# Performance work log

Measured on AMD Instinct MI355X. Metric: run time of the kernel, lower is better.

Reference implementation:

```python
import jax, jax.numpy as jnp
import numpy as np

# ---- hyperparameters (from init_kwargs) ----
B, SEQ, D_MODEL = 2, 2048, 1024
D_STATE, D_CONV, EXPAND, HEAD_DIM, CHUNK = 128, 4, 2, 64, 256
D_INNER = EXPAND * D_MODEL            # 2048
NH = D_INNER // HEAD_DIM              # 32 heads
CONV_DIM = D_INNER + 2 * D_STATE      # 2304
D_IN_PROJ = 2 * D_INNER + 2 * D_STATE + NH  # z, xBC, dt -> 4384
D_FF = 4 * D_MODEL
EPS = 1e-12


def setup_inputs() -> dict:
    key = jax.random.key(0)
    ks = jax.random.split(key, 16)
    s = 0.02
    f32 = jnp.float32
    inp = {
        "x": jax.random.normal(ks[0], (B, SEQ, D_MODEL), f32),
        "time_diff": jax.random.uniform(ks[1], (B, SEQ), f32),
        # TiSSD (Mamba2-style) params
        "W_in": jax.random.normal(ks[2], (D_MODEL, D_IN_PROJ), f32) * s,
        "b_in": jnp.zeros((D_IN_PROJ,), f32),
        "conv_w": jax.random.normal(ks[3], (CONV_DIM, D_CONV), f32) * s,
        "conv_b": jnp.zeros((CONV_DIM,), f32),
        "A_log": jnp.log(jnp.arange(1, NH + 1, dtype=f32)),
        "dt_bias": jnp.full((NH,), -2.0, f32),
        "D": jnp.ones((NH,), f32),
        "time_decay": jnp.full((NH,), -3.0, f32),   # time-aware decay rates
        "rms_w": jnp.ones((D_INNER,), f32),
        "W_out": jax.random.normal(ks[4], (D_INNER, D_MODEL), f32) * s,
        "b_out": jnp.zeros((D_MODEL,), f32),
        # wrapper LayerNorm
        "ln_g": jnp.ones((D_MODEL,), f32),
        "ln_b": jnp.zeros((D_MODEL,), f32),
        # FFN
        "fc1_w": jax.random.normal(ks[5], (D_MODEL, D_FF), f32) * s,
        "fc1_b": jnp.zeros((D_FF,), f32),
        "fc2_w": jax.random.normal(ks[6], (D_FF, D_MODEL), f32) * s,
        "fc2_b": jnp.zeros((D_MODEL,), f32),
        "ln2_g": jnp.ones((D_MODEL,), f32),
        "ln2_b": jnp.zeros((D_MODEL,), f32),
    }
    return inp


def _layer_norm(x, g, b, eps=EPS):
    mu = jnp.mean(x, axis=-1, keepdims=True)
    var = jnp.mean(jnp.square(x - mu), axis=-1, keepdims=True)
    return (x - mu) * jax.lax.rsqrt(var + eps) * g + b


def _hardswish(x):
    return x * jnp.clip(x + 3.0, 0.0, 6.0) * (1.0 / 6.0)


def _tissd_forward(x, time_diff, W_in, b_in, conv_w, conv_b, A_log, dt_bias, D,
                   time_decay, rms_w, W_out, b_out):
    b, l, _ = x.shape
    zxbcdt = x @ W_in + b_in                       # [b,l,D_IN_PROJ]
    z = zxbcdt[..., :D_INNER]
    xBC = zxbcdt[..., D_INNER:D_INNER + CONV_DIM]
    dt_raw = zxbcdt[..., -NH:]

    # causal depthwise conv1d (small fixed kernel -> unrolled shifts)
    xp = jnp.pad(xBC, ((0, 0), (D_CONV - 1, 0), (0, 0)))
    xBC_c = conv_b
    for k in range(D_CONV):
        xBC_c = xBC_c + xp[:, k:k + l, :] * conv_w[:, k]
    xBC_c = jax.nn.silu(xBC_c)

    xs = xBC_c[..., :D_INNER]
    Bm = xBC_c[..., D_INNER:D_INNER + D_STATE]     # [b,l,n]
    Cm = xBC_c[..., -D_STATE:]                     # [b,l,n]

    dt = jax.nn.softplus(dt_raw + dt_bias)         # [b,l,h]
    A = -jnp.exp(A_log)                            # [h]
    # time-aware: extra decay proportional to time gap
    dA = dt * A - jax.nn.softplus(time_decay) * time_diff[..., None]  # [b,l,h]

    xh = xs.reshape(b, l, NH, HEAD_DIM)
    xdt = xh * dt[..., None]                       # [b,l,h,p]

    nc = l // CHUNK
    xc = xdt.reshape(b, nc, CHUNK, NH, HEAD_DIM)
    Bc = Bm.reshape(b, nc, CHUNK, D_STATE)
    Cc = Cm.reshape(b, nc, CHUNK, D_STATE)
    dAc = dA.reshape(b, nc, CHUNK, NH).transpose(0, 3, 1, 2)  # [b,h,c,L]

    A_cum = jnp.cumsum(dAc, axis=-1)               # [b,h,c,L]
    seg = A_cum[..., :, None] - A_cum[..., None, :]
    mask = jnp.tril(jnp.ones((CHUNK, CHUNK), bool))
    Lmat = jnp.where(mask, jnp.exp(jnp.where(mask, seg, 0.0)), 0.0)  # [b,h,c,L,L]

    # intra-chunk (diagonal block) output
    Y_diag = jnp.einsum("bcln,bcsn,bhcls,bcshp->bclhp", Cc, Bc, Lmat, xc)

    # per-chunk final states
    decay_states = jnp.exp(A_cum[..., -1:] - A_cum)  # [b,h,c,L]
    states = jnp.einsum("bcln,bhcl,bclhp->bchpn", Bc, decay_states, xc)
    chunk_decay = jnp.exp(A_cum[..., -1])            # [b,h,c]

    # inter-chunk recurrence over nc chunks
    states_t = states.transpose(1, 0, 2, 3, 4)       # [c,b,h,p,n]
    decay_t = chunk_decay.transpose(2, 0, 1)         # [c,b,h]

    def step(carry, inp):
        s_c, d_c = inp
        new = carry * d_c[..., None, None] + s_c
        return new, carry                            # emit state BEFORE chunk

    init = jnp.zeros((b, NH, HEAD_DIM, D_STATE), x.dtype)
    _, prev_states = jax.lax.scan(step, init, (states_t, decay_t))
    prev_states = prev_states.transpose(1, 0, 2, 3, 4)  # [b,c,h,p,n]

    state_decay = jnp.exp(A_cum)                     # [b,h,c,L]
    Y_off = jnp.einsum("bcln,bchpn,bhcl->bclhp", Cc, prev_states, state_decay)

    Y = (Y_diag + Y_off).reshape(b, l, NH, HEAD_DIM) + D[None, None, :, None] * xh
    y = Y.reshape(b, l, D_INNER)

    # gated RMSNorm
    y = y * jax.nn.silu(z)
    y = y * jax.lax.rsqrt(jnp.mean(jnp.square(y), axis=-1, keepdims=True) + EPS) * rms_w
    return y @ W_out + b_out


def reference(x, time_diff, W_in, b_in, conv_w, conv_b, A_log, dt_bias, D,
              time_decay, rms_w, W_out, b_out, ln_g, ln_b,
              fc1_w, fc1_b, fc2_w, fc2_b, ln2_g, ln2_b):
    hidden = _tissd_forward(x, time_diff, W_in, b_in, conv_w, conv_b, A_log,
                            dt_bias, D, time_decay, rms_w, W_out, b_out)
    # num_layers > 1 -> residual; dropout is identity in eval mode
    h = _layer_norm(hidden + x, ln_g, ln_b)
    # FFN with Hardswish and residual LayerNorm
    hid = _hardswish(h @ fc1_w + fc1_b)
    hid = hid @ fc2_w + fc2_b
    out = _layer_norm(hid + h, ln2_g, ln2_b)
    return (out, time_diff)
```

## Files before the change

kernel.cpp:

```cpp
#include <hip/hip_runtime.h>

#define BATCH 2
#define SEQL 2048
#define DM 1024
#define DSTATE 128
#define HD 64
#define CHUNK 256
#define DI 2048
#define NHEADS 32
#define CONVD 2304
#define DPROJ 4384
#define DFF 4096
#define NC 8
#define ROWS (BATCH*SEQL)

typedef unsigned short ushort_t;
typedef short bf16x8 __attribute__((ext_vector_type(8)));
typedef float f32x4 __attribute__((ext_vector_type(4)));

__device__ __forceinline__ float softplus_f(float v){
    return (v > 20.f) ? v : log1pf(expf(v));
}
__device__ __forceinline__ float silu_f(float v){
    return v / (1.f + expf(-v));
}
__device__ __forceinline__ ushort_t f2b(float v){
    union { float f; unsigned int u; } x; x.f = v;
    unsigned int r = x.u + 0x7fffu + ((x.u >> 16) & 1u);
    return (ushort_t)(r >> 16);
}
__device__ __forceinline__ float b2f(ushort_t v){
    union { unsigned int u; float f; } x; x.u = ((unsigned int)v) << 16;
    return x.f;
}

template<int ACT, int OUT_BF16, int TN, int NS, int DTX>
__global__ __launch_bounds__(256) void mfma_gemm_k(
    const ushort_t* __restrict__ A, const ushort_t* __restrict__ Bt,
    const float* __restrict__ bias, float* __restrict__ Cf,
    ushort_t* __restrict__ Cb, float* __restrict__ dtaux,
    int M, int N, int K, int ldc)
{
    constexpr int NT = (TN == 128) ? 4 : 2;
    constexpr int BROWS = TN / 4;
    __shared__ ushort_t As[128*64];
    __shared__ ushort_t Bs[TN*64];
    int tid = threadIdx.x;
    int lane = tid & 63, wave = tid >> 6;
    int m0 = blockIdx.y * 128, n0 = blockIdx.x * TN;
    int Ks = K / NS;
    int kb = (NS > 1) ? blockIdx.z * Ks : 0;
    int wave_m = (TN==128) ? (wave >> 1)*64 : (wave & 1)*64;
    int wave_n = (TN==128) ? (wave & 1)*64 : (wave >> 1)*32;
    int lrow = lane >> 3;
    int lcol = ((lane & 7) ^ lrow) * 8;
    const ushort_t* Abase = A  + (size_t)(m0 + wave*32    + lrow)*K + lcol + kb;
    const ushort_t* Bbase = Bt + (size_t)(n0 + wave*BROWS + lrow)*K + lcol + kb;
    ushort_t* AsW = &As[(wave*32)*64];
    ushort_t* BsW = &Bs[(wave*BROWS)*64];
    f32x4 acc[4][NT];
    #pragma unroll
    for (int i=0;i<4;i++)
        #pragma unroll
        for (int j=0;j<NT;j++) acc[i][j] = (f32x4){0.f,0.f,0.f,0.f};
    int lm = lane & 15;
    int quad = lane >> 4;
    for (int k0 = 0; k0 < Ks; k0 += 64){
        #pragma unroll
        for (int j = 0; j < 4; j++)
            __builtin_amdgcn_global_load_lds(
                (const __attribute__((address_space(1))) void*)(Abase + (size_t)(j*8)*K + k0),
                (__attribute__((address_space(3))) void*)(AsW + j*8*64), 16, 0, 0);
        #pragma unroll
        for (int j = 0; j < BROWS/8; j++)
            __builtin_amdgcn_global_load_lds(
                (const __attribute__((address_space(1))) void*)(Bbase + (size_t)(j*8)*K + k0),
                (__attribute__((address_space(3))) void*)(BsW + j*8*64), 16, 0, 0);
        __syncthreads();
        #pragma unroll
        for (int kk = 0; kk < 64; kk += 32){
            int cb = kk >> 3;
            bf16x8 af[4], bfr[NT];
            #pragma unroll
            for (int mt=0; mt<4; mt++)
                af[mt] = *(const bf16x8*)&As[(wave_m + mt*16 + lm)*64 + (((cb + quad) ^ (lm & 7))*8)];
            #pragma unroll
            for (int nt=0; nt<NT; nt++)
                bfr[nt] = *(const bf16x8*)&Bs[(wave_n + nt*16 + lm)*64 + (((cb + quad) ^ (lm & 7))*8)];
            #pragma unroll
            for (int mt=0; mt<4; mt++)
                #pragma unroll
                for (int nt=0; nt<NT; nt++)
                    acc[mt][nt] = __builtin_amdgcn_mfma_f32_16x16x32_bf16(af[mt], bfr[nt], acc[mt][nt], 0, 0, 0);
        }
        __syncthreads();
    }
    float* Cfo = Cf + (size_t)((NS > 1) ? blockIdx.z : 0) * (size_t)M * ldc;
    int addb = (NS == 1) || (blockIdx.z == 0);
    int crow0 = m0 + wave_m + quad * 4;
    int ccol0 = n0 + wave_n + lm;
    #pragma unroll
    for (int mt=0; mt<4; mt++){
        #pragma unroll
        for (int nt=0; nt<NT; nt++){
            int col = ccol0 + nt*16;
            if (col < N){
                float bv = addb ? bias[col] : 0.f;
                #pragma unroll
                for (int r=0; r<4; r++){
                    int row = crow0 + mt*16 + r;
                    float v = acc[mt][nt][r] + bv;
                    if (ACT == 1){
                        float t = fminf(fmaxf(v + 3.f, 0.f), 6.f);
                        v = v * t * (1.f/6.f);
                    }
                    if (OUT_BF16){
                        Cb[(size_t)row*ldc + col] = f2b(v);
                        if (DTX && col >= N - NHEADS)
                            dtaux[(size_t)row*NHEADS + (col - (N - NHEADS))] = v;
                    } else {
                        Cfo[(size_t)row*ldc + col] = v;
                    }
                }
            }
        }
    }
}

__global__ __launch_bounds__(256) void transpose_bf_k(const float* __restrict__ W,
                                                      ushort_t* __restrict__ Wt,
                                                      int K, int N){
    __shared__ ushort_t tile[32][33];
    int n0 = blockIdx.x*32, k0 = blockIdx.y*32;
    int tx = threadIdx.x & 31, ty = threadIdx.x >> 5;
    #pragma unroll
    for (int i = 0; i < 4; i++){
        int k = k0 + ty + i*8;
        int n = n0 + tx;
        float v = (n < N) ? W[(size_t)k*N + n] : 0.f;
        tile[ty + i*8][tx] = f2b(v);
    }
    __syncthreads();
    #pragma unroll
    for (int i = 0; i < 4; i++){
        Wt[(size_t)(n0 + ty + i*8)*K + k0 + tx] = tile[tx][ty + i*8];
    }
}

__global__ __launch_bounds__(256) void f2b_k(const float* __restrict__ in,
                                             ushort_t* __restrict__ outp, int n){
    int idx = blockIdx.x*256 + threadIdx.x;
    if (idx < n) outp[idx] = f2b(in[idx]);
}

__global__ __launch_bounds__(256) void conv_silu_k(const ushort_t* __restrict__ zx,
                                                   const float* __restrict__ conv_w,
                                                   const float* __restrict__ conv_b,
                                                   const float* __restrict__ dt,
                                                   float* __restrict__ convb,
                                                   float* __restrict__ xdt){
    int idx = blockIdx.x*256 + threadIdx.x;
    int c = idx % CONVD;
    int row = idx / CONVD;
    int t = row & (SEQL-1);
    float acc = conv_b[c];
    #pragma unroll
    for (int k = 0; k < 4; k++){
        int tt = t + k - 3;
        if (tt >= 0)
            acc += b2f(zx[((size_t)(row + k - 3))*DPROJ + DI + c]) * conv_w[c*4 + k];
    }
    float v = silu_f(acc);
    convb[idx] = v;
    if (c < DI)
        xdt[(size_t)row*DI + c] = v * dt[(size_t)row*NHEADS + (c >> 6)];
}

__global__ __launch_bounds__(256) void dt_scan_k(const float* __restrict__ dtaux,
                                                 const float* __restrict__ time_diff,
                                                 const float* __restrict__ A_log,
                                                 const float* __restrict__ dt_bias,
                                                 const float* __restrict__ time_decay,
                                                 float* __restrict__ dt_out,
                                                 float* __restrict__ Acum){
    __shared__ float s[CHUNK];
    int bid = blockIdx.x;
    int c = bid % NC;
    int h = (bid / NC) % NHEADS;
    int b = bid / (NC*NHEADS);
    int l = threadIdx.x;
    int t = c*CHUNK + l;
    float dtr = dtaux[((size_t)(b*SEQL + t))*NHEADS + h];
    float dtv = softplus_f(dtr + dt_bias[h]);
    float A = -expf(A_log[h]);
    float dA = dtv*A - softplus_f(time_decay[h]) * time_diff[b*SEQL + t];
    dt_out[(size_t)(b*SEQL + t)*NHEADS + h] = dtv;
    s[l] = dA;
    __syncthreads();
    for (int off = 1; off < CHUNK; off <<= 1){
        float v = (l >= off) ? s[l-off] : 0.f;
        __syncthreads();
        s[l] += v;
        __syncthreads();
    }
    Acum[((size_t)(b*NHEADS + h))*SEQL + t] = s[l];
}

__global__ __launch_bounds__(256) void g_mfma_k(const float* __restrict__ convb,
                                                float* __restrict__ G){
    __shared__ ushort_t As[64*136];
    __shared__ ushort_t Bs[64*136];
    int bc = blockIdx.z;
    int l0 = blockIdx.y*64, s0 = blockIdx.x*64;
    int tid = threadIdx.x;
    int lane = tid & 63, wave = tid >> 6;
    int lm = lane & 15, quad = lane >> 4;
    const float* base = convb + (size_t)bc*CHUNK*CONVD;
    #pragma unroll
    for (int i = 0; i < 32; i++){
        int e = tid + i*256; int r = e >> 7, k = e & 127;
        As[r*136 + k] = f2b(base[(size_t)(l0+r)*CONVD + DI + DSTATE + k]);
        Bs[r*136 + k] = f2b(base[(size_t)(s0+r)*CONVD + DI + k]);
    }
    __syncthreads();
    f32x4 acc[4];
    #pragma unroll
    for (int j=0;j<4;j++) acc[j] = (f32x4){0.f,0.f,0.f,0.f};
    #pragma unroll
    for (int kk = 0; kk < 4; kk++){
        bf16x8 af = *(const bf16x8*)&As[(wave*16+lm)*136 + kk*32 + quad*8];
        #pragma unroll
        for (int nt = 0; nt < 4; nt++){
            bf16x8 bfr = *(const bf16x8*)&Bs[(nt*16+lm)*136 + kk*32 + quad*8];
            acc[nt] = __builtin_amdgcn_mfma_f32_16x16x32_bf16(af, bfr, acc[nt], 0, 0, 0);
        }
    }
    float* g = G + (size_t)bc*CHUNK*CHUNK;
    #pragma unroll
    for (int nt = 0; nt < 4; nt++)
        #pragma unroll
        for (int r = 0; r < 4; r++)
            g[(size_t)(l0 + wave*16 + quad*4 + r)*CHUNK + s0 + nt*16 + lm] = acc[nt][r];
}

#define RSX 264
#define RSB 72
__global__ __launch_bounds__(256) void states_mfma_k(const float* __restrict__ convb,
                                                     const float* __restrict__ xdt,
                                                     const float* __restrict__ Acum,
                                                     float* __restrict__ states){
    __shared__ ushort_t xw[64*RSX];
    __shared__ ushort_t Bt[128*RSB];
    __shared__ float Acs[CHUNK];
    int bid = blockIdx.x;
    int h = bid % NHEADS;
    int c = (bid / NHEADS) % NC;
    int b = bid / (NHEADS*NC);
    int tid = threadIdx.x;
    int lane = tid & 63, wave = tid >> 6;
    int lm = lane & 15, quad = lane >> 4;
    Acs[tid] = Acum[((size_t)(b*NHEADS + h))*SEQL + c*CHUNK + tid];
    __syncthreads();
    float AcL = Acs[CHUNK-1];
    {
        const float* xg = xdt + ((size_t)(b*SEQL + c*CHUNK))*DI + h*HD;
        #pragma unroll
        for (int j8 = 0; j8 < 8; j8++){
            int s0 = wave*64 + j8*8;
            bf16x8 pk;
            #pragma unroll
            for (int j = 0; j < 8; j++)
                pk[j] = (short)f2b(expf(AcL - Acs[s0+j]) * xg[(size_t)(s0+j)*DI + lane]);
            *(bf16x8*)&xw[lane*RSX + s0] = pk;
        }
    }
    f32x4 acc[8];
    #pragma unroll
    for (int j=0;j<8;j++) acc[j] = (f32x4){0.f,0.f,0.f,0.f};
    const float* bbase = convb + ((size_t)(b*SEQL + c*CHUNK))*CONVD + DI;
    for (int l0 = 0; l0 < CHUNK; l0 += 64){
        __syncthreads();
        #pragma unroll
        for (int i = 0; i < 32; i++){
            int e = tid + i*256; int l = e >> 7, n = e & 127;
            Bt[n*RSB + l] = f2b(bbase[(size_t)(l0+l)*CONVD + n]);
        }
        __syncthreads();
        #pragma unroll
        for (int kk = 0; kk < 2; kk++){
            bf16x8 af = *(const bf16x8*)&xw[(wave*16+lm)*RSX + l0 + kk*32 + quad*8];
            #pragma unroll
            for (int nt = 0; nt < 8; nt++){
                bf16x8 bfr = *(const bf16x8*)&Bt[(nt*16+lm)*RSB + kk*32 + quad*8];
                acc[nt] = __builtin_amdgcn_mfma_f32_16x16x32_bf16(af, bfr, acc[nt], 0, 0, 0);
            }
        }
    }
    float* outp = states + ((size_t)((b*NC + c)*NHEADS + h))*(HD*DSTATE);
    #pragma unroll
    for (int nt = 0; nt < 8; nt++)
        #pragma unroll
        for (int r = 0; r < 4; r++)
            outp[(size_t)(wave*16 + quad*4 + r)*DSTATE + nt*16 + lm] = acc[nt][r];
}

__global__ __launch_bounds__(256) void prev_scan_k(const float* __restrict__ states,
                                                   const float* __restrict__ Acum,
                                                   float* __restrict__ prev){
    int bid = blockIdx.x;
    int h = bid % NHEADS, b = bid / NHEADS;
    int tid = threadIdx.x;
    const float* AcB = Acum + ((size_t)(b*NHEADS + h))*SEQL;
    float dec[NC];
    #pragma unroll
    for (int c = 0; c < NC; c++) dec[c] = expf(AcB[c*CHUNK + CHUNK-1]);
    for (int j = 0; j < 32; j++){
        int e = tid + j*256;
        float carry = 0.f;
        #pragma unroll
        for (int c = 0; c < NC; c++){
            size_t idx = ((size_t)((b*NC + c)*NHEADS + h))*(HD*DSTATE) + e;
            prev[idx] = carry;
            carry = carry*dec[c] + states[idx];
        }
    }
}

#define RLX 264
#define RLP 136
__global__ __launch_bounds__(256) void y_mfma_k(const float* __restrict__ convb,
                                                const float* __restrict__ G,
                                                const float* __restrict__ Acum,
                                                const float* __restrict__ prev,
                                                const float* __restrict__ Dp,
                                                float* __restrict__ Y){
    __shared__ ushort_t xdtT[64*RLX];
    __shared__ ushort_t prevs[64*RLP];
    __shared__ float Acs[CHUNK];
    int bid = blockIdx.x;
    int h = bid % NHEADS;
    int c = (bid / NHEADS) % NC;
    int b = bid / (NHEADS*NC);
    int tid = threadIdx.x;
    int lane = tid & 63, wave = tid >> 6;
    int lm = lane & 15, quad = lane >> 4;

    Acs[tid] = Acum[((size_t)(b*NHEADS + h))*SEQL + c*CHUNK + tid];
    {
        const float* pv = prev + ((size_t)((b*NC + c)*NHEADS + h))*(HD*DSTATE);
        #pragma unroll
        for (int i = 0; i < 32; i++){
            int e = tid + i*256; int p = e >> 7, n = e & 127;
            prevs[p*RLP + n] = f2b(pv[e]);
        }
    }
    {
        const float* xg = Y + ((size_t)(b*SEQL + c*CHUNK))*DI + h*HD;
        #pragma unroll
        for (int j8 = 0; j8 < 8; j8++){
            int s0 = wave*64 + j8*8;
            bf16x8 pk;
            #pragma unroll
            for (int j = 0; j < 8; j++)
                pk[j] = (short)f2b(xg[(size_t)(s0+j)*DI + lane]);
            *(bf16x8*)&xdtT[lane*RLX + s0] = pk;
        }
    }
    __syncthreads();

    int   lrow[4];  float Alr[4], eAlr[4];
    #pragma unroll
    for (int mt = 0; mt < 4; mt++){
        lrow[mt] = (mt*4 + wave)*16 + lm;
        Alr[mt]  = Acs[lrow[mt]];
        eAlr[mt] = expf(Alr[mt]);
    }
    const float* Gbase = G + ((size_t)(b*NC + c))*(CHUNK*CHUNK);

    f32x4 acc[4][4];
    #pragma unroll
    for (int i=0;i<4;i++)
        #pragma unroll
        for (int j=0;j<4;j++) acc[i][j] = (f32x4){0.f,0.f,0.f,0.f};

    for (int ks = 0; ks < 8; ks++){
        bf16x8 bfr[4];
        #pragma unroll
        for (int nt = 0; nt < 4; nt++)
            bfr[nt] = *(const bf16x8*)&xdtT[(nt*16+lm)*RLX + ks*32 + quad*8];
        #pragma unroll
        for (int mt = 0; mt < 4; mt++){
            int rblk = mt*4 + wave;
            int nst = rblk/2 + 1;
            if (ks < nst){
                int sbase = ks*32 + quad*8;
                const float4* G4 = (const float4*)(Gbase + (size_t)lrow[mt]*CHUNK + sbase);
                float4 g0 = G4[0], g1 = G4[1];
                const float4* A4 = (const float4*)(&Acs[sbase]);
                float4 a0 = A4[0], a1 = A4[1];
                float Al = Alr[mt]; int l = lrow[mt];
                float pv[8];
                pv[0] = (sbase+0 <= l) ? g0.x*expf(Al - a0.x) : 0.f;
                pv[1] = (sbase+1 <= l) ? g0.y*expf(Al - a0.y) : 0.f;
                pv[2] = (sbase+2 <= l) ? g0.z*expf(Al - a0.z) : 0.f;
                pv[3] = (sbase+3 <= l) ? g0.w*expf(Al - a0.w) : 0.f;
                pv[4] = (sbase+4 <= l) ? g1.x*expf(Al - a1.x) : 0.f;
                pv[5] = (sbase+5 <= l) ? g1.y*expf(Al - a1.y) : 0.f;
                pv[6] = (sbase+6 <= l) ? g1.z*expf(Al - a1.z) : 0.f;
                pv[7] = (sbase+7 <= l) ? g1.w*expf(Al - a1.w) : 0.f;
                bf16x8 af;
                #pragma unroll
                for (int j = 0; j < 8; j++) af[j] = (short)f2b(pv[j]);
                #pragma unroll
                for (int nt = 0; nt < 4; nt++)
                    acc[mt][nt] = __builtin_amdgcn_mfma_f32_16x16x32_bf16(af, bfr[nt], acc[mt][nt], 0, 0, 0);
            }
        }
    }
    for (int kc = 0; kc < 4; kc++){
        bf16x8 bfr[4];
        #pragma unroll
        for (int nt = 0; nt < 4; nt++)
            bfr[nt] = *(const bf16x8*)&prevs[(nt*16+lm)*RLP + kc*32 + quad*8];
        #pragma unroll
        for (int mt = 0; mt < 4; mt++){
            int rowg = b*SEQL + c*CHUNK + lrow[mt];
            const float4* C4 = (const float4*)(convb + (size_t)rowg*CONVD + DI + DSTATE + kc*32 + quad*8);
            float4 c0 = C4[0], c1 = C4[1];
            float e = eAlr[mt];
            bf16x8 af;
            af[0] = (short)f2b(e*c0.x); af[1] = (short)f2b(e*c0.y);
            af[2] = (short)f2b(e*c0.z); af[3] = (short)f2b(e*c0.w);
            af[4] = (short)f2b(e*c1.x); af[5] = (short)f2b(e*c1.y);
            af[6] = (short)f2b(e*c1.z); af[7] = (short)f2b(e*c1.w);
            #pragma unroll
            for (int nt = 0; nt < 4; nt++)
                acc[mt][nt] = __builtin_amdgcn_mfma_f32_16x16x32_bf16(af, bfr[nt], acc[mt][nt], 0, 0, 0);
        }
    }
    float Dv = Dp[h];
    #pragma unroll
    for (int mt = 0; mt < 4; mt++){
        int l0 = (mt*4 + wave)*16 + quad*4;
        #pragma unroll
        for (int nt = 0; nt < 4; nt++){
            int p = nt*16 + lm;
            #pragma unroll
            for (int r = 0; r < 4; r++){
                int rowg = b*SEQL + c*CHUNK + l0 + r;
                float xs = convb[(size_t)rowg*CONVD + h*HD + p];
                Y[(size_t)rowg*DI + h*HD + p] = acc[mt][nt][r] + Dv*xs;
            }
        }
    }
}

__global__ __launch_bounds__(256) void gate_rms_k(const float* __restrict__ Yb,
                                                  const ushort_t* __restrict__ zx,
                                                  const float* __restrict__ rms_w,
                                                  ushort_t* __restrict__ yn){
    __shared__ float red[4];
    __shared__ float scale_s;
    int row = blockIdx.x; int tid = threadIdx.x;
    float v[8]; float ss = 0.f;
    #pragma unroll
    for (int i = 0; i < 8; i++){
        int d = tid + i*256;
        float g = Yb[(size_t)row*DI + d] * silu_f(b2f(zx[(size_t)row*DPROJ + d]));
        v[i] = g; ss += g*g;
    }
    #pragma unroll
    for (int off = 32; off > 0; off >>= 1) ss += __shfl_down(ss, off);
    int lane = tid & 63, wid = tid >> 6;
    if (lane == 0) red[wid] = ss;
    __syncthreads();
    if (tid == 0) scale_s = rsqrtf((red[0]+red[1]+red[2]+red[3])*(1.f/DI) + 1e-12f);
    __syncthreads();
    float sc = scale_s;
    #pragma unroll
    for (int i = 0; i < 8; i++){
        int d = tid + i*256;
        yn[(size_t)row*DI + d] = f2b(v[i]*sc*rms_w[d]);
    }
}

template<int WB, int TWO>
__global__ __launch_bounds__(256) void ln_k(const float* __restrict__ a,
                                            const float* __restrict__ a2,
                                            const float* __restrict__ resid,
                                            const float* __restrict__ g,
                                            const float* __restrict__ bw,
                                            float* __restrict__ outp,
                                            ushort_t* __restrict__ bfout){
    __shared__ float redA[4], redB[4];
    __shared__ float mu_s, rs_s;
    int row = blockIdx.x; int tid = threadIdx.x;
    float u[4]; float s = 0.f, s2 = 0.f;
    #pragma unroll
    for (int i = 0; i < 4; i++){
        int d = tid + i*256;
        float val = a[(size_t)row*DM + d] + resid[(size_t)row*DM + d];
        if (TWO) val += a2[(size_t)row*DM + d];
        u[i] = val; s += val; s2 += val*val;
    }
    #pragma unroll
    for (int off = 32; off > 0; off >>= 1){
        s  += __shfl_down(s,  off);
        s2 += __shfl_down(s2, off);
    }
    int lane = tid & 63, wid = tid >> 6;
    if (lane == 0){ redA[wid] = s; redB[wid] = s2; }
    __syncthreads();
    if (tid == 0){
        float S  = redA[0]+redA[1]+redA[2]+redA[3];
        float S2 = redB[0]+redB[1]+redB[2]+redB[3];
        float mu = S*(1.f/DM);
        float var = S2*(1.f/DM) - mu*mu;
        mu_s = mu; rs_s = rsqrtf(var + 1e-12f);
    }
    __syncthreads();
    float mu = mu_s, rs = rs_s;
    #pragma unroll
    for (int i = 0; i < 4; i++){
        int d = tid + i*256;
        float o = (u[i]-mu)*rs*g[d] + bw[d];
        outp[(size_t)row*DM + d] = o;
        if (WB) bfout[(size_t)row*DM + d] = f2b(o);
    }
}

__global__ __launch_bounds__(256) void copy_td_k(const float* __restrict__ td,
                                                 float* __restrict__ outp){
    int idx = blockIdx.x*256 + threadIdx.x;
    outp[idx] = td[idx];
}

extern "C" void kernel_launch(void* const* d_in, const int* in_sizes, int n_in,
                              void* d_out, int out_size, void* d_ws, size_t ws_size,
                              hipStream_t stream){
    const float* x         = (const float*)d_in[0];
    const float* time_diff = (const float*)d_in[1];
    const float* W_in      = (const float*)d_in[2];
    const float* b_in      = (const float*)d_in[3];
    const float* conv_w    = (const float*)d_in[4];
    const float* conv_b    = (const float*)d_in[5];
    const float* A_log     = (const float*)d_in[6];
    const float* dt_bias   = (const float*)d_in[7];
    const float* Dp        = (const float*)d_in[8];
    const float* time_dec  = (const float*)d_in[9];
    const float* rms_w     = (const float*)d_in[10];
    const float* W_out     = (const float*)d_in[11];
    const float* b_out     = (const float*)d_in[12];
    const float* ln_g      = (const float*)d_in[13];
    const float* ln_b      = (const float*)d_in[14];
    const float* fc1_w     = (const float*)d_in[15];
    const float* fc1_b     = (const float*)d_in[16];
    const float* fc2_w     = (const float*)d_in[17];
    const float* fc2_b     = (const float*)d_in[18];
    const float* ln2_g     = (const float*)d_in[19];
    const float* ln2_b     = (const float*)d_in[20];

    float* ws = (float*)d_ws;
    float* zx    = ws;
    float* convb = zx    + 17956864;
    float* dt    = convb + 9437184;
    float* Acum  = dt    + 131072;
    float* xdt   = Acum  + 131072;
    float* r5    = xdt   + 8388608;
    float* hbuf  = r5    + 9437184;
    ushort_t* zx_bf  = (ushort_t*)zx;
    float*    dtaux  = zx + 10600000;
    ushort_t* mid_bf = (ushort_t*)zx;
    ushort_t* h_bf   = (ushort_t*)(zx + 8388608);
    ushort_t* x_bf  = (ushort_t*)xdt;
    ushort_t* WinT  = (ushort_t*)(xdt + 2097152);
    ushort_t* WoutT = (ushort_t*)(xdt + 4194304);
    float* fc2Pa = xdt;
    float* Gbuf = r5;
    float* stat = r5 + 1048576;
    float* prev = stat + 4194304;
    ushort_t* yn_bf = (ushort_t*)r5;
    ushort_t* fc1T  = (ushort_t*)(r5 + 4194304);
    ushort_t* fc2T  = (ushort_t*)(r5 + 6291456);
    float* outPa  = convb;
    float* outp   = (float*)d_out;

    f2b_k<<<(ROWS*DM)/256, 256, 0, stream>>>(x, x_bf, ROWS*DM);
    transpose_bf_k<<<dim3(4480/32, DM/32), 256, 0, stream>>>(W_in, WinT, DM, DPROJ);
    mfma_gemm_k<0,1,128,1,1><<<dim3(35, ROWS/128), 256, 0, stream>>>(x_bf, WinT, b_in, nullptr, zx_bf, dtaux, ROWS, DPROJ, DM, DPROJ);
    dt_scan_k<<<BATCH*NHEADS*NC, 256, 0, stream>>>(dtaux, time_diff, A_log, dt_bias, time_dec, dt, Acum);
    conv_silu_k<<<ROWS*CONVD/256, 256, 0, stream>>>(zx_bf, conv_w, conv_b, dt, convb, xdt);
    g_mfma_k<<<dim3(4,4,BATCH*NC), 256, 0, stream>>>(convb, Gbuf);
    states_mfma_k<<<BATCH*NC*NHEADS, 256, 0, stream>>>(convb, xdt, Acum, stat);
    prev_scan_k<<<BATCH*NHEADS, 256, 0, stream>>>(stat, Acum, prev);
    y_mfma_k<<<BATCH*NC*NHEADS, 256, 0, stream>>>(convb, Gbuf, Acum, prev, Dp, xdt);
    gate_rms_k<<<ROWS, 256, 0, stream>>>(xdt, zx_bf, rms_w, yn_bf);
    transpose_bf_k<<<dim3(DM/32, DI/32), 256, 0, stream>>>(W_out, WoutT, DI, DM);
    mfma_gemm_k<0,0,64,2,0><<<dim3(DM/64, ROWS/128, 2), 256, 0, stream>>>(yn_bf, WoutT, b_out, outPa, nullptr, nullptr, ROWS, DM, DI, DM);
    ln_k<1,1><<<ROWS, 256, 0, stream>>>(outPa, outPa + (size_t)ROWS*DM, x, ln_g, ln_b, hbuf, h_bf);
    transpose_bf_k<<<dim3(DFF/32, DM/32), 256, 0, stream>>>(fc1_w, fc1T, DM, DFF);
    transpose_bf_k<<<dim3(DM/32, DFF/32), 256, 0, stream>>>(fc2_w, fc2T, DFF, DM);
    mfma_gemm_k<1,1,128,1,0><<<dim3(DFF/128, ROWS/128), 256, 0, stream>>>(h_bf, fc1T, fc1_b, nullptr, mid_bf, nullptr, ROWS, DFF, DM, DFF);
    mfma_gemm_k<0,0,64,2,0><<<dim3(DM/64, ROWS/128, 2), 256, 0, stream>>>(mid_bf, fc2T, fc2_b, fc2Pa, nullptr, nullptr, ROWS, DM, DFF, DM);
    ln_k<0,1><<<ROWS, 256, 0, stream>>>(fc2Pa, fc2Pa + (size_t)ROWS*DM, hbuf, ln2_g, ln2_b, outp, nullptr);
    copy_td_k<<<ROWS/256, 256, 0, stream>>>(time_diff, outp + (size_t)ROWS*DM);
}
```

Measured before the change: 523.8 us.

## Store SSD intermediates in bf16 and merge small prep/epilogue launches

Stores the conv output, the G matrix and Y in bf16 instead of fp32, which cuts memory traffic in the SSD kernels and allows vectorized bf16x8 loads. It also merges the x cast with the W_in transpose, the three weight transposes into one launch, and the time_diff copy into the final LayerNorm, so fewer kernels are launched. The first LayerNorm now writes only a bf16 copy, and the final LayerNorm reads that as its residual. This saves bandwidth but adds rounding error to the residual path and to the SSD intermediates.

```diff
diff --git a/kernel.cpp b/kernel.cpp
--- a/kernel.cpp
+++ b/kernel.cpp
@@ -127,37 +127,64 @@
     }
 }
 
-__global__ __launch_bounds__(256) void transpose_bf_k(const float* __restrict__ W,
-                                                      ushort_t* __restrict__ Wt,
-                                                      int K, int N){
+__global__ __launch_bounds__(256) void prep_in_k(const float* __restrict__ x,
+                                                 ushort_t* __restrict__ x_bf,
+                                                 const float* __restrict__ W_in,
+                                                 ushort_t* __restrict__ WinT){
     __shared__ ushort_t tile[32][33];
-    int n0 = blockIdx.x*32, k0 = blockIdx.y*32;
+    int bid = blockIdx.x;
+    if (bid < 16384){
+        int idx = bid*256 + threadIdx.x;
+        x_bf[idx] = f2b(x[idx]);
+        return;
+    }
+    int id2 = bid - 16384;
+    int n0 = (id2 % 140)*32, k0 = (id2 / 140)*32;
     int tx = threadIdx.x & 31, ty = threadIdx.x >> 5;
     #pragma unroll
     for (int i = 0; i < 4; i++){
         int k = k0 + ty + i*8;
         int n = n0 + tx;
-        float v = (n < N) ? W[(size_t)k*N + n] : 0.f;
+        float v = (n < DPROJ) ? W_in[(size_t)k*DPROJ + n] : 0.f;
         tile[ty + i*8][tx] = f2b(v);
     }
     __syncthreads();
     #pragma unroll
+    for (int i = 0; i < 4; i++)
+        WinT[(size_t)(n0 + ty + i*8)*DM + k0 + tx] = tile[tx][ty + i*8];
+}
+
+__global__ __launch_bounds__(256) void transpose3_k(const float* __restrict__ Wout,
+                                                    const float* __restrict__ fc1w,
+                                                    const float* __restrict__ fc2w,
+                                                    ushort_t* __restrict__ WoutT,
+                                                    ushort_t* __restrict__ fc1T,
+                                                    ushort_t* __restrict__ fc2T){
+    __shared__ ushort_t tile[32][33];
+    int bid = blockIdx.x;
+    const float* W; ushort_t* Wt; int K, N, gx, id;
+    if (bid < 2048){        W = Wout; Wt = WoutT; K = DI;  N = DM;  gx = 32;  id = bid; }
+    else if (bid < 6144){   W = fc1w; Wt = fc1T;  K = DM;  N = DFF; gx = 128; id = bid - 2048; }
+    else {                  W = fc2w; Wt = fc2T;  K = DFF; N = DM;  gx = 32;  id = bid - 6144; }
+    int n0 = (id % gx)*32, k0 = (id / gx)*32;
+    int tx = threadIdx.x & 31, ty = threadIdx.x >> 5;
+    #pragma unroll
     for (int i = 0; i < 4; i++){
+        int k = k0 + ty + i*8;
+        int n = n0 + tx;
+        tile[ty + i*8][tx] = f2b(W[(size_t)k*N + n]);
+    }
+    __syncthreads();
+    #pragma unroll
+    for (int i = 0; i < 4; i++)
         Wt[(size_t)(n0 + ty + i*8)*K + k0 + tx] = tile[tx][ty + i*8];
-    }
-}
-
-__global__ __launch_bounds__(256) void f2b_k(const float* __restrict__ in,
-                                             ushort_t* __restrict__ outp, int n){
-    int idx = blockIdx.x*256 + threadIdx.x;
-    if (idx < n) outp[idx] = f2b(in[idx]);
 }
 
 __global__ __launch_bounds__(256) void conv_silu_k(const ushort_t* __restrict__ zx,
                                                    const float* __restrict__ conv_w,
                                                    const float* __restrict__ conv_b,
                                                    const float* __restrict__ dt,
-                                                   float* __restrict__ convb,
+                                                   ushort_t* __restrict__ convb,
                                                    float* __restrict__ xdt){
     int idx = blockIdx.x*256 + threadIdx.x;
     int c = idx % CONVD;
@@ -171,7 +198,7 @@
             acc += b2f(zx[((size_t)(row + k - 3))*DPROJ + DI + c]) * conv_w[c*4 + k];
     }
     float v = silu_f(acc);
-    convb[idx] = v;
+    convb[idx] = f2b(v);
     if (c < DI)
         xdt[(size_t)row*DI + c] = v * dt[(size_t)row*NHEADS + (c >> 6)];
 }
@@ -206,8 +233,8 @@
     Acum[((size_t)(b*NHEADS + h))*SEQL + t] = s[l];
 }
 
-__global__ __launch_bounds__(256) void g_mfma_k(const float* __restrict__ convb,
-                                                float* __restrict__ G){
+__global__ __launch_bounds__(256) void g_mfma_k(const ushort_t* __restrict__ convb,
+                                                ushort_t* __restrict__ G){
     __shared__ ushort_t As[64*136];
     __shared__ ushort_t Bs[64*136];
     int bc = blockIdx.z;
@@ -215,12 +242,13 @@
     int tid = threadIdx.x;
     int lane = tid & 63, wave = tid >> 6;
     int lm = lane & 15, quad = lane >> 4;
-    const float* base = convb + (size_t)bc*CHUNK*CONVD;
-    #pragma unroll
-    for (int i = 0; i < 32; i++){
-        int e = tid + i*256; int r = e >> 7, k = e & 127;
-        As[r*136 + k] = f2b(base[(size_t)(l0+r)*CONVD + DI + DSTATE + k]);
-        Bs[r*136 + k] = f2b(base[(size_t)(s0+r)*CONVD + DI + k]);
+    const ushort_t* base = convb + (size_t)bc*CHUNK*CONVD;
+    #pragma unroll
+    for (int i = 0; i < 4; i++){
+        int e = tid + i*256;
+        int r = e >> 4, k = (e & 15)*8;
+        *(bf16x8*)&As[r*136 + k] = *(const bf16x8*)&base[(size_t)(l0+r)*CONVD + DI + DSTATE + k];
+        *(bf16x8*)&Bs[r*136 + k] = *(const bf16x8*)&base[(size_t)(s0+r)*CONVD + DI + k];
     }
     __syncthreads();
     f32x4 acc[4];
@@ -235,17 +263,17 @@
             acc[nt] = __builtin_amdgcn_mfma_f32_16x16x32_bf16(af, bfr, acc[nt], 0, 0, 0);
         }
     }
-    float* g = G + (size_t)bc*CHUNK*CHUNK;
+    ushort_t* g = G + (size_t)bc*CHUNK*CHUNK;
     #pragma unroll
     for (int nt = 0; nt < 4; nt++)
         #pragma unroll
         for (int r = 0; r < 4; r++)
-            g[(size_t)(l0 + wave*16 + quad*4 + r)*CHUNK + s0 + nt*16 + lm] = acc[nt][r];
+            g[(size_t)(l0 + wave*16 + quad*4 + r)*CHUNK + s0 + nt*16 + lm] = f2b(acc[nt][r]);
 }
 
 #define RSX 264
 #define RSB 72
-__global__ __launch_bounds__(256) void states_mfma_k(const float* __restrict__ convb,
+__global__ __launch_bounds__(256) void states_mfma_k(const ushort_t* __restrict__ convb,
                                                      const float* __restrict__ xdt,
                                                      const float* __restrict__ Acum,
                                                      float* __restrict__ states){
@@ -277,13 +305,13 @@
     f32x4 acc[8];
     #pragma unroll
     for (int j=0;j<8;j++) acc[j] = (f32x4){0.f,0.f,0.f,0.f};
-    const float* bbase = convb + ((size_t)(b*SEQL + c*CHUNK))*CONVD + DI;
+    const ushort_t* bbase = convb + ((size_t)(b*SEQL + c*CHUNK))*CONVD + DI;
     for (int l0 = 0; l0 < CHUNK; l0 += 64){
         __syncthreads();
         #pragma unroll
         for (int i = 0; i < 32; i++){
             int e = tid + i*256; int l = e >> 7, n = e & 127;
-            Bt[n*RSB + l] = f2b(bbase[(size_t)(l0+l)*CONVD + n]);
+            Bt[n*RSB + l] = bbase[(size_t)(l0+l)*CONVD + n];
         }
         __syncthreads();
         #pragma unroll
@@ -328,12 +356,13 @@
 
 #define RLX 264
 #define RLP 136
-__global__ __launch_bounds__(256) void y_mfma_k(const float* __restrict__ convb,
-                                                const float* __restrict__ G,
+__global__ __launch_bounds__(256) void y_mfma_k(const ushort_t* __restrict__ convb,
+                                                const ushort_t* __restrict__ G,
                                                 const float* __restrict__ Acum,
                                                 const float* __restrict__ prev,
                                                 const float* __restrict__ Dp,
-                                                float* __restrict__ Y){
+                                                const float* __restrict__ xdt,
+                                                ushort_t* __restrict__ Ybf){
     __shared__ ushort_t xdtT[64*RLX];
     __shared__ ushort_t prevs[64*RLP];
     __shared__ float Acs[CHUNK];
@@ -355,7 +384,7 @@
         }
     }
     {
-        const float* xg = Y + ((size_t)(b*SEQL + c*CHUNK))*DI + h*HD;
+        const float* xg = xdt + ((size_t)(b*SEQL + c*CHUNK))*DI + h*HD;
         #pragma unroll
         for (int j8 = 0; j8 < 8; j8++){
             int s0 = wave*64 + j8*8;
@@ -375,7 +404,7 @@
         Alr[mt]  = Acs[lrow[mt]];
         eAlr[mt] = expf(Alr[mt]);
     }
-    const float* Gbase = G + ((size_t)(b*NC + c))*(CHUNK*CHUNK);
+    const ushort_t* Gbase = G + ((size_t)(b*NC + c))*(CHUNK*CHUNK);
 
     f32x4 acc[4][4];
     #pragma unroll
@@ -394,20 +423,19 @@
             int nst = rblk/2 + 1;
             if (ks < nst){
                 int sbase = ks*32 + quad*8;
-                const float4* G4 = (const float4*)(Gbase + (size_t)lrow[mt]*CHUNK + sbase);
-                float4 g0 = G4[0], g1 = G4[1];
+                bf16x8 g8 = *(const bf16x8*)&Gbase[(size_t)lrow[mt]*CHUNK + sbase];
                 const float4* A4 = (const float4*)(&Acs[sbase]);
                 float4 a0 = A4[0], a1 = A4[1];
                 float Al = Alr[mt]; int l = lrow[mt];
                 float pv[8];
-                pv[0] = (sbase+0 <= l) ? g0.x*expf(Al - a0.x) : 0.f;
-                pv[1] = (sbase+1 <= l) ? g0.y*expf(Al - a0.y) : 0.f;
-                pv[2] = (sbase+2 <= l) ? g0.z*expf(Al - a0.z) : 0.f;
-                pv[3] = (sbase+3 <= l) ? g0.w*expf(Al - a0.w) : 0.f;
-                pv[4] = (sbase+4 <= l) ? g1.x*expf(Al - a1.x) : 0.f;
-                pv[5] = (sbase+5 <= l) ? g1.y*expf(Al - a1.y) : 0.f;
-                pv[6] = (sbase+6 <= l) ? g1.z*expf(Al - a1.z) : 0.f;
-                pv[7] = (sbase+7 <= l) ? g1.w*expf(Al - a1.w) : 0.f;
+                pv[0] = (sbase+0 <= l) ? b2f((ushort_t)g8[0])*expf(Al - a0.x) : 0.f;
+                pv[1] = (sbase+1 <= l) ? b2f((ushort_t)g8[1])*expf(Al - a0.y) : 0.f;
+                pv[2] = (sbase+2 <= l) ? b2f((ushort_t)g8[2])*expf(Al - a0.z) : 0.f;
+                pv[3] = (sbase+3 <= l) ? b2f((ushort_t)g8[3])*expf(Al - a0.w) : 0.f;
+                pv[4] = (sbase+4 <= l) ? b2f((ushort_t)g8[4])*expf(Al - a1.x) : 0.f;
+                pv[5] = (sbase+5 <= l) ? b2f((ushort_t)g8[5])*expf(Al - a1.y) : 0.f;
+                pv[6] = (sbase+6 <= l) ? b2f((ushort_t)g8[6])*expf(Al - a1.z) : 0.f;
+                pv[7] = (sbase+7 <= l) ? b2f((ushort_t)g8[7])*expf(Al - a1.w) : 0.f;
                 bf16x8 af;
                 #pragma unroll
                 for (int j = 0; j < 8; j++) af[j] = (short)f2b(pv[j]);
@@ -425,14 +453,11 @@
         #pragma unroll
         for (int mt = 0; mt < 4; mt++){
             int rowg = b*SEQL + c*CHUNK + lrow[mt];
-            const float4* C4 = (const float4*)(convb + (size_t)rowg*CONVD + DI + DSTATE + kc*32 + quad*8);
-            float4 c0 = C4[0], c1 = C4[1];
+            bf16x8 c8 = *(const bf16x8*)&convb[(size_t)rowg*CONVD + DI + DSTATE + kc*32 + quad*8];
             float e = eAlr[mt];
             bf16x8 af;
-            af[0] = (short)f2b(e*c0.x); af[1] = (short)f2b(e*c0.y);
-            af[2] = (short)f2b(e*c0.z); af[3] = (short)f2b(e*c0.w);
-            af[4] = (short)f2b(e*c1.x); af[5] = (short)f2b(e*c1.y);
-            af[6] = (short)f2b(e*c1.z); af[7] = (short)f2b(e*c1.w);
+            #pragma unroll
+            for (int j = 0; j < 8; j++) af[j] = (short)f2b(e * b2f((ushort_t)c8[j]));
             #pragma unroll
             for (int nt = 0; nt < 4; nt++)
                 acc[mt][nt] = __builtin_amdgcn_mfma_f32_16x16x32_bf16(af, bfr[nt], acc[mt][nt], 0, 0, 0);
@@ -448,14 +473,14 @@
             #pragma unroll
             for (int r = 0; r < 4; r++){
                 int rowg = b*SEQL + c*CHUNK + l0 + r;
-                float xs = convb[(size_t)rowg*CONVD + h*HD + p];
-                Y[(size_t)rowg*DI + h*HD + p] = acc[mt][nt][r] + Dv*xs;
+                float xs = b2f(convb[(size_t)rowg*CONVD + h*HD + p]);
+                Ybf[(size_t)rowg*DI + h*HD + p] = f2b(acc[mt][nt][r] + Dv*xs);
             }
         }
     }
 }
 
-__global__ __launch_bounds__(256) void gate_rms_k(const float* __restrict__ Yb,
+__global__ __launch_bounds__(256) void gate_rms_k(const ushort_t* __restrict__ Yb,
                                                   const ushort_t* __restrict__ zx,
                                                   const float* __restrict__ rms_w,
                                                   ushort_t* __restrict__ yn){
@@ -466,7 +491,7 @@
     #pragma unroll
     for (int i = 0; i < 8; i++){
         int d = tid + i*256;
-        float g = Yb[(size_t)row*DI + d] * silu_f(b2f(zx[(size_t)row*DPROJ + d]));
+        float g = b2f(Yb[(size_t)row*DI + d]) * silu_f(b2f(zx[(size_t)row*DPROJ + d]));
         v[i] = g; ss += g*g;
     }
     #pragma unroll
@@ -484,14 +509,12 @@
     }
 }
 
-template<int WB, int TWO>
-__global__ __launch_bounds__(256) void ln_k(const float* __restrict__ a,
-                                            const float* __restrict__ a2,
-                                            const float* __restrict__ resid,
-                                            const float* __restrict__ g,
-                                            const float* __restrict__ bw,
-                                            float* __restrict__ outp,
-                                            ushort_t* __restrict__ bfout){
+__global__ __launch_bounds__(256) void ln_hbf_k(const float* __restrict__ a,
+                                                const float* __restrict__ a2,
+                                                const float* __restrict__ resid,
+                                                const float* __restrict__ g,
+                                                const float* __restrict__ bw,
+                                                ushort_t* __restrict__ bfout){
     __shared__ float redA[4], redB[4];
     __shared__ float mu_s, rs_s;
     int row = blockIdx.x; int tid = threadIdx.x;
@@ -499,8 +522,7 @@
     #pragma unroll
     for (int i = 0; i < 4; i++){
         int d = tid + i*256;
-        float val = a[(size_t)row*DM + d] + resid[(size_t)row*DM + d];
-        if (TWO) val += a2[(size_t)row*DM + d];
+        float val = a[(size_t)row*DM + d] + a2[(size_t)row*DM + d] + resid[(size_t)row*DM + d];
         u[i] = val; s += val; s2 += val*val;
     }
     #pragma unroll
@@ -523,16 +545,54 @@
     #pragma unroll
     for (int i = 0; i < 4; i++){
         int d = tid + i*256;
-        float o = (u[i]-mu)*rs*g[d] + bw[d];
-        outp[(size_t)row*DM + d] = o;
-        if (WB) bfout[(size_t)row*DM + d] = f2b(o);
-    }
-}
-
-__global__ __launch_bounds__(256) void copy_td_k(const float* __restrict__ td,
-                                                 float* __restrict__ outp){
-    int idx = blockIdx.x*256 + threadIdx.x;
-    outp[idx] = td[idx];
+        bfout[(size_t)row*DM + d] = f2b((u[i]-mu)*rs*g[d] + bw[d]);
+    }
+}
+
+__global__ __launch_bounds__(256) void ln_final_k(const float* __restrict__ a,
+                                                  const float* __restrict__ a2,
+                                                  const ushort_t* __restrict__ residb,
+                                                  const float* __restrict__ g,
+                                                  const float* __restrict__ bw,
+                                                  float* __restrict__ outp,
+                                                  const float* __restrict__ td){
+    __shared__ float redA[4], redB[4];
+    __shared__ float mu_s, rs_s;
+    int row = blockIdx.x; int tid = threadIdx.x;
+    if (row >= ROWS){
+        int idx = (row - ROWS)*256 + tid;
+        outp[(size_t)ROWS*DM + idx] = td[idx];
+        return;
+    }
+    float u[4]; float s = 0.f, s2 = 0.f;
+    #pragma unroll
+    for (int i = 0; i < 4; i++){
+        int d = tid + i*256;
+        float val = a[(size_t)row*DM + d] + a2[(size_t)row*DM + d] + b2f(residb[(size_t)row*DM + d]);
+        u[i] = val; s += val; s2 += val*val;
+    }
+    #pragma unroll
+    for (int off = 32; off > 0; off >>= 1){
+        s  += __shfl_down(s,  off);
+        s2 += __shfl_down(s2, off);
+    }
+    int lane = tid & 63, wid = tid >> 6;
+    if (lane == 0){ redA[wid] = s; redB[wid] = s2; }
+    __syncthreads();
+    if (tid == 0){
+        float S  = redA[0]+redA[1]+redA[2]+redA[3];
+        float S2 = redB[0]+redB[1]+redB[2]+redB[3];
+        float mu = S*(1.f/DM);
+        float var = S2*(1.f/DM) - mu*mu;
+        mu_s = mu; rs_s = rsqrtf(var + 1e-12f);
+    }
+    __syncthreads();
+    float mu = mu_s, rs = rs_s;
+    #pragma unroll
+    for (int i = 0; i < 4; i++){
+        int d = tid + i*256;
+        outp[(size_t)row*DM + d] = (u[i]-mu)*rs*g[d] + bw[d];
+    }
 }
 
 extern "C" void kernel_launch(void* const* d_in, const int* in_sizes, int n_in,
@@ -567,41 +627,39 @@
     float* Acum  = dt    + 131072;
     float* xdt   = Acum  + 131072;
     float* r5    = xdt   + 8388608;
-    float* hbuf  = r5    + 9437184;
+    float* ybreg = r5    + 9437184;
     ushort_t* zx_bf  = (ushort_t*)zx;
     float*    dtaux  = zx + 10600000;
     ushort_t* mid_bf = (ushort_t*)zx;
     ushort_t* h_bf   = (ushort_t*)(zx + 8388608);
+    ushort_t* convb_bf = (ushort_t*)convb;
+    float* outPa  = convb;
     ushort_t* x_bf  = (ushort_t*)xdt;
     ushort_t* WinT  = (ushort_t*)(xdt + 2097152);
     ushort_t* WoutT = (ushort_t*)(xdt + 4194304);
     float* fc2Pa = xdt;
-    float* Gbuf = r5;
+    ushort_t* Gb   = (ushort_t*)r5;
     float* stat = r5 + 1048576;
     float* prev = stat + 4194304;
     ushort_t* yn_bf = (ushort_t*)r5;
     ushort_t* fc1T  = (ushort_t*)(r5 + 4194304);
     ushort_t* fc2T  = (ushort_t*)(r5 + 6291456);
-    float* outPa  = convb;
+    ushort_t* Ybf = (ushort_t*)ybreg;
     float* outp   = (float*)d_out;
 
-    f2b_k<<<(ROWS*DM)/256, 256, 0, stream>>>(x, x_bf, ROWS*DM);
-    transpose_bf_k<<<dim3(4480/32, DM/32), 256, 0, stream>>>(W_in, WinT, DM, DPROJ);
+    prep_in_k<<<16384 + 4480, 256, 0, stream>>>(x, x_bf, W_in, WinT);
     mfma_gemm_k<0,1,128,1,1><<<dim3(35, ROWS/128), 256, 0, stream>>>(x_bf, WinT, b_in, nullptr, zx_bf, dtaux, ROWS, DPROJ, DM, DPROJ);
     dt_scan_k<<<BATCH*NHEADS*NC, 256, 0, stream>>>(dtaux, time_diff, A_log, dt_bias, time_dec, dt, Acum);
-    conv_silu_k<<<ROWS*CONVD/256, 256, 0, stream>>>(zx_bf, conv_w, conv_b, dt, convb, xdt);
-    g_mfma_k<<<dim3(4,4,BATCH*NC), 256, 0, stream>>>(convb, Gbuf);
-    states_mfma_k<<<BATCH*NC*NHEADS, 256, 0, stream>>>(convb, xdt, Acum, stat);
+    conv_silu_k<<<ROWS*CONVD/256, 256, 0, stream>>>(zx_bf, conv_w, conv_b, dt, convb_bf, xdt);
+    g_mfma_k<<<dim3(4,4,BATCH*NC), 256, 0, stream>>>(convb_bf, Gb);
+    states_mfma_k<<<BATCH*NC*NHEADS, 256, 0, stream>>>(convb_bf, xdt, Acum, stat);
     prev_scan_k<<<BATCH*NHEADS, 256, 0, stream>>>(stat, Acum, prev);
-    y_mfma_k<<<BATCH*NC*NHEADS, 256, 0, stream>>>(convb, Gbuf, Acum, prev, Dp, xdt);
-    gate_rms_k<<<ROWS, 256, 0, stream>>>(xdt, zx_bf, rms_w, yn_bf);
-    transpose_bf_k<<<dim3(DM/32, DI/32), 256, 0, stream>>>(W_out, WoutT, DI, DM);
+    y_mfma_k<<<BATCH*NC*NHEADS, 256, 0, stream>>>(convb_bf, Gb, Acum, prev, Dp, xdt, Ybf);
+    gate_rms_k<<<ROWS, 256, 0, stream>>>(Ybf, zx_bf, rms_w, yn_bf);
+    transpose3_k<<<10240, 256, 0, stream>>>(W_out, fc1_w, fc2_w, WoutT, fc1T, fc2T);
     mfma_gemm_k<0,0,64,2,0><<<dim3(DM/64, ROWS/128, 2), 256, 0, stream>>>(yn_bf, WoutT, b_out, outPa, nullptr, nullptr, ROWS, DM, DI, DM);
-    ln_k<1,1><<<ROWS, 256, 0, stream>>>(outPa, outPa + (size_t)ROWS*DM, x, ln_g, ln_b, hbuf, h_bf);
-    transpose_bf_k<<<dim3(DFF/32, DM/32), 256, 0, stream>>>(fc1_w, fc1T, DM, DFF);
-    transpose_bf_k<<<dim3(DM/32, DFF/32), 256, 0, stream>>>(fc2_w, fc2T, DFF, DM);
+    ln_hbf_k<<<ROWS, 256, 0, stream>>>(outPa, outPa + (size_t)ROWS*DM, x, ln_g, ln_b, h_bf);
     mfma_gemm_k<1,1,128,1,0><<<dim3(DFF/128, ROWS/128), 256, 0, stream>>>(h_bf, fc1T, fc1_b, nullptr, mid_bf, nullptr, ROWS, DFF, DM, DFF);
     mfma_gemm_k<0,0,64,2,0><<<dim3(DM/64, ROWS/128, 2), 256, 0, stream>>>(mid_bf, fc2T, fc2_b, fc2Pa, nullptr, nullptr, ROWS, DM, DFF, DM);
-    ln_k<0,1><<<ROWS, 256, 0, stream>>>(fc2Pa, fc2Pa + (size_t)ROWS*DM, hbuf, ln2_g, ln2_b, outp, nullptr);
-    copy_td_k<<<ROWS/256, 256, 0, stream>>>(time_diff, outp + (size_t)ROWS*DM);
-}
+    ln_final_k<<<ROWS + ROWS/256, 256, 0, stream>>>(fc2Pa, fc2Pa + (size_t)ROWS*DM, h_bf, ln2_g, ln2_b, outp, time_diff);
+}
```

Result: faster. 504.9 us (-3.6%).
